# Optimization experiments

Measured on AMD Instinct MI355X. Metric: run time of the kernel, lower is better.

The kernel has to match this reference:

```python
import jax, jax.numpy as jnp
import numpy as np

# 3x3 hexagon kernel mask: zero at (0,2) and (2,0), matching HexagonConv2d
_KM = np.ones((3, 3), np.float32)
_KM[0, 2] = 0.0
_KM[2, 0] = 0.0
KMASK = jnp.asarray(_KM)


def _out_mask():
    # static 13x13 mask encoding the post-conv zeroing loops
    m = np.ones((13, 13), np.float32)
    for i in range(5):
        for j in range(8 + i, 13):
            m[i, j] = 0.0
    for i in range(4):
        m[2 + i, 9 + i] = 0.0
    m[6:9, 12] = 0.0
    for i in range(6):
        for j in range(i + 1):
            m[6 + i, j] = 0.0
    for i in range(3):
        m[5 + i, 0 + i] = 0.0
    m[3:5, 0] = 0.0
    return jnp.asarray(m)

OUT_MASK = _out_mask()


def _hex_pad(x):
    # x: [B,C,13,13] -> zero-pad to [B,C,15,15], then hexagonal wraparound copies.
    # Copies applied sequentially, exactly matching the torch in-place order
    # (one copy, row 0 <- row 12, feeds a later read at (0,7)).
    x = jnp.pad(x, ((0, 0), (0, 0), (1, 1), (1, 1)))
    r2 = jnp.arange(2)
    r3 = jnp.arange(3)
    r4 = jnp.arange(4)
    r8 = jnp.arange(8)
    x = x.at[:, :, 0, 1:8].set(x[:, :, 12, 7:14])
    x = x.at[:, :, r3, 8 + r3].set(x[:, :, 6 + r3, 2 + r3])
    x = x.at[:, :, 3 + r4, 10 + r4].set(x[:, :, 9 + r4, 4 + r4])
    x = x.at[:, :, 7 + r3, 13].set(x[:, :, 1 + r3, 1])
    x = x.at[:, :, 10 + r3, 14].set(x[:, :, 4 + r3, 2])
    x = x.at[:, :, 13, 7 + r8].set(x[:, :, 1, 1 + r8])
    x = x.at[:, :, 9 + r4, 3 + r4].set(x[:, :, 3 + r4, 9 + r4])
    x = x.at[:, :, 6 + r3, 1 + r3].set(x[:, :, r3, 7 + r3])
    x = x.at[:, :, 4 + r2, 1].set(x[:, :, 10 + r2, 13])
    x = x.at[:, :, r4, 0].set(x[:, :, 6 + r4, 12])
    return x


def setup_inputs() -> dict:
    key = jax.random.key(0)
    kx, kw, kb = jax.random.split(key, 3)
    B, Cin, Cout, H = 4096, 64, 64, 13
    x = jax.random.normal(kx, (B, Cin, H, H), dtype=jnp.float32)
    fan_in = Cin * 9
    w = jax.random.normal(kw, (Cout, Cin, 3, 3), dtype=jnp.float32) / np.sqrt(fan_in)
    b = jax.random.normal(kb, (Cout,), dtype=jnp.float32) * 0.01
    return {"x": x, "w": w, "b": b}


def reference(x, w, b):
    xp = _hex_pad(x)                      # [B,C,15,15]
    wm = w * KMASK                        # hexagonal kernel mask
    y = jax.lax.conv_general_dilated(
        xp, wm, window_strides=(1, 1), padding="VALID",
        dimension_numbers=("NCHW", "OIHW", "NCHW"))  # [B,Cout,13,13]
    y = y + b[None, :, None, None]
    return y * OUT_MASK
```

## Files before the change

### kernel.cpp

```cpp
#include <hip/hip_runtime.h>
#include <stdint.h>

typedef __attribute__((ext_vector_type(8))) short short8;
typedef __attribute__((ext_vector_type(4))) float float4v;

#define NPIX 240
#define PIXSTRIDE 68

#define MAP_OFF   57344
#define OM_OFF    58304

__device__ __forceinline__ unsigned short f2bf(float f) {
    union { float f; unsigned u; } v; v.f = f;
    unsigned r = v.u + 0x7FFFu + ((v.u >> 16) & 1u);
    return (unsigned short)(r >> 16);
}

__global__ void hex_prep_kernel(const float* __restrict__ w,
                                unsigned short* __restrict__ wsA,
                                int* __restrict__ map,
                                float* __restrict__ om) {
    const int gid = blockIdx.x * blockDim.x + threadIdx.x;
    const int nthr = gridDim.x * blockDim.x;
    const int ti_tab[7] = {0,0,1,1,1,2,2};
    const int tj_tab[7] = {0,1,0,1,2,1,2};
    for (int item = gid; item < 4*14*64; item += nthr) {
        int lane = item & 63;
        int ks   = (item >> 6) % 14;
        int ct   = (item >> 6) / 14;
        int co = ct*16 + (lane & 15);
        int k0 = ks*32 + (lane >> 4)*8;
        unsigned short vals[8];
        #pragma unroll
        for (int j = 0; j < 8; ++j) {
            int k = k0 + j;
            int tap = k >> 6, ci = k & 63;
            vals[j] = f2bf(w[(co*64 + ci)*9 + ti_tab[tap]*3 + tj_tab[tap]]);
        }
        for (int j = 0; j < 8; ++j) wsA[item*8 + j] = vals[j];
    }
    if (gid == 0) {
        int m[225];
        for (int r = 0; r < 15; ++r)
            for (int c = 0; c < 15; ++c)
                m[r*15+c] = (r>=1 && r<=13 && c>=1 && c<=13) ? (r-1)*13 + (c-1) : -1;
        #define M(r,c) m[(r)*15+(c)]
        for (int t = 0; t < 7; ++t) M(0,1+t)    = M(12,7+t);
        for (int r = 0; r < 3; ++r) M(r,8+r)    = M(6+r,2+r);
        for (int r = 0; r < 4; ++r) M(3+r,10+r) = M(9+r,4+r);
        for (int r = 0; r < 3; ++r) M(7+r,13)   = M(1+r,1);
        for (int r = 0; r < 3; ++r) M(10+r,14)  = M(4+r,2);
        for (int r = 0; r < 8; ++r) M(13,7+r)   = M(1,1+r);
        for (int r = 0; r < 4; ++r) M(9+r,3+r)  = M(3+r,9+r);
        for (int r = 0; r < 3; ++r) M(6+r,1+r)  = M(r,7+r);
        for (int r = 0; r < 2; ++r) M(4+r,1)    = M(10+r,13);
        for (int r = 0; r < 4; ++r) M(r,0)      = M(6+r,12);
        #undef M
        for (int i = 0; i < 225; ++i) map[i] = m[i];
        for (int i = 225; i < 240; ++i) map[i] = -1;
        float o[169];
        for (int i = 0; i < 169; ++i) o[i] = 1.f;
        for (int i = 0; i < 5; ++i) for (int j = 8+i; j < 13; ++j) o[i*13+j] = 0.f;
        for (int i = 0; i < 4; ++i) o[(2+i)*13 + 9+i] = 0.f;
        for (int i = 6; i < 9; ++i) o[i*13 + 12] = 0.f;
        for (int i = 0; i < 6; ++i) for (int j = 0; j <= i; ++j) o[(6+i)*13 + j] = 0.f;
        for (int i = 0; i < 3; ++i) o[(5+i)*13 + i] = 0.f;
        o[3*13 + 0] = 0.f; o[4*13 + 0] = 0.f;
        for (int i = 0; i < 169; ++i) om[i] = o[i];
    }
}

__global__ __launch_bounds__(256, 2) void hexconv_kernel(
        const float* __restrict__ x, const float* __restrict__ bias,
        const unsigned short* __restrict__ wsA, const int* __restrict__ map,
        const float* __restrict__ om, float* __restrict__ out) {
    __shared__ unsigned short Xs[NPIX * PIXSTRIDE];
    const int b   = blockIdx.x;
    const int tid = threadIdx.x;
    const int lane = tid & 63, wv = tid >> 6;
    const int lr = lane & 15, lq = lane >> 4;
    const float* xb = x + (size_t)b * 64 * 169;

    const int ctp = wv & 1;
    const int nth = wv >> 1;

    short8 afr[2][14];
    #pragma unroll
    for (int c = 0; c < 2; ++c) {
        const int ct = ctp*2 + c;
        #pragma unroll
        for (int ks = 0; ks < 14; ++ks)
            afr[c][ks] = *(const short8*)(wsA + (size_t)((ct*14 + ks)*64 + lane)*8);
    }

    int sp[4];
    #pragma unroll
    for (int pi = 0; pi < 4; ++pi) {
        int pix = lane + 64*pi;
        sp[pi] = (pix < NPIX) ? map[pix] : -1;
    }
    #pragma unroll
    for (int pi = 0; pi < 4; ++pi) {
        int pix = lane + 64*pi;
        if (pix < NPIX) {
            const int s = sp[pi];
            unsigned short vals[16];
            #pragma unroll
            for (int cj = 0; cj < 16; ++cj) {
                int ci = wv*16 + cj;
                float v = (s >= 0) ? xb[ci*169 + s] : 0.f;
                vals[cj] = f2bf(v);
            }
            #pragma unroll
            for (int q = 0; q < 4; ++q) {
                uint64_t pk = (uint64_t)vals[4*q]
                            | ((uint64_t)vals[4*q+1] << 16)
                            | ((uint64_t)vals[4*q+2] << 32)
                            | ((uint64_t)vals[4*q+3] << 48);
                *(uint64_t*)&Xs[pix*PIXSTRIDE + wv*16 + q*4] = pk;
            }
        }
    }
    __syncthreads();

    float4v acc[2][7];
    #pragma unroll
    for (int c = 0; c < 2; ++c)
        #pragma unroll
        for (int j = 0; j < 7; ++j)
            acc[c][j] = float4v{0.f, 0.f, 0.f, 0.f};

    const int offs[7] = {0,1,15,16,17,31,32};
    #pragma unroll
    for (int ks = 0; ks < 14; ++ks) {
        const int tap = ks >> 1;
        const int cib = (ks & 1)*32 + lq*8;
        #pragma unroll
        for (int j = 0; j < 7; ++j) {
            int nt = nth*7 + j;
            if (nt < 13) {
                int pixb = nt*16 + lr + offs[tap];
                const unsigned short* p = &Xs[pixb*PIXSTRIDE + cib];
                union { short8 v; uint64_t q[2]; } u;
                u.q[0] = *(const uint64_t*)p;
                u.q[1] = *(const uint64_t*)(p + 4);
                #pragma unroll
                for (int c = 0; c < 2; ++c)
                    acc[c][j] = __builtin_amdgcn_mfma_f32_16x16x32_bf16(
                        afr[c][ks], u.v, acc[c][j], 0, 0, 0);
            }
        }
    }

    #pragma unroll
    for (int j = 0; j < 7; ++j) {
        int nt = nth*7 + j;
        if (nt >= 13) continue;
        int p15 = nt*16 + lr;
        int y = p15 / 15, xc = p15 % 15;
        if (xc >= 13 || y >= 13) continue;
        float omv = om[y*13 + xc];
        size_t obase = (size_t)b*64*169 + y*13 + xc;
        #pragma unroll
        for (int c = 0; c < 2; ++c) {
            int ct = ctp*2 + c;
            #pragma unroll
            for (int r = 0; r < 4; ++r) {
                int co = ct*16 + lq*4 + r;
                out[obase + (size_t)co*169] = (acc[c][j][r] + bias[co]) * omv;
            }
        }
    }
}

extern "C" void kernel_launch(void* const* d_in, const int* in_sizes, int n_in,
                              void* d_out, int out_size, void* d_ws, size_t ws_size,
                              hipStream_t stream) {
    const float* x    = (const float*)d_in[0];
    const float* w    = (const float*)d_in[1];
    const float* bias = (const float*)d_in[2];
    float* out = (float*)d_out;

    unsigned short* wsA = (unsigned short*)d_ws;
    int*   map = (int*)((char*)d_ws + MAP_OFF);
    float* om  = (float*)((char*)d_ws + OM_OFF);

    hex_prep_kernel<<<16, 256, 0, stream>>>(w, wsA, map, om);

    int B = in_sizes[0] / (64 * 169);
    hexconv_kernel<<<B, 256, 0, stream>>>(x, bias, wsA, map, om, out);
}
```

Baseline: 358.8 us.

## Make conv kernel persistent with double-buffered LDS prefetch of next image

Switches from one block per image to 512 persistent blocks, each processing a contiguous chunk of images. Weight fragments, bias, pixel maps and output mask are loaded once per block, and the next image's global loads and bf16 LDS writes are interleaved with the MFMA work on the current image using two LDS buffers. The aim is to hide global load latency behind compute and to amortize per-block setup. It doubles LDS use, which may reduce occupancy, and raises register pressure from holding the prefetched values.

```diff
diff --git a/kernel.cpp b/kernel.cpp
--- a/kernel.cpp
+++ b/kernel.cpp
@@ -1,5 +1,6 @@
 #include <hip/hip_runtime.h>
 #include <stdint.h>
+
 
 typedef __attribute__((ext_vector_type(8))) short short8;
 typedef __attribute__((ext_vector_type(4))) float float4v;
@@ -73,17 +74,19 @@
 __global__ __launch_bounds__(256, 2) void hexconv_kernel(
         const float* __restrict__ x, const float* __restrict__ bias,
         const unsigned short* __restrict__ wsA, const int* __restrict__ map,
-        const float* __restrict__ om, float* __restrict__ out) {
-    __shared__ unsigned short Xs[NPIX * PIXSTRIDE];
-    const int b   = blockIdx.x;
+        const float* __restrict__ om, float* __restrict__ out,
+        int B, int ipb) {
+    __shared__ unsigned short Xs[2][NPIX * PIXSTRIDE];
     const int tid = threadIdx.x;
     const int lane = tid & 63, wv = tid >> 6;
     const int lr = lane & 15, lq = lane >> 4;
-    const float* xb = x + (size_t)b * 64 * 169;
-
     const int ctp = wv & 1;
     const int nth = wv >> 1;
 
+    const int b0   = blockIdx.x * ipb;
+    const int bend = (b0 + ipb < B) ? (b0 + ipb) : B;
+    if (b0 >= bend) return;
+
     short8 afr[2][14];
     #pragma unroll
     for (int c = 0; c < 2; ++c) {
@@ -92,85 +95,143 @@
         for (int ks = 0; ks < 14; ++ks)
             afr[c][ks] = *(const short8*)(wsA + (size_t)((ct*14 + ks)*64 + lane)*8);
     }
-
     int sp[4];
     #pragma unroll
     for (int pi = 0; pi < 4; ++pi) {
         int pix = lane + 64*pi;
         sp[pi] = (pix < NPIX) ? map[pix] : -1;
     }
-    #pragma unroll
-    for (int pi = 0; pi < 4; ++pi) {
-        int pix = lane + 64*pi;
-        if (pix < NPIX) {
-            const int s = sp[pi];
-            unsigned short vals[16];
-            #pragma unroll
-            for (int cj = 0; cj < 16; ++cj) {
-                int ci = wv*16 + cj;
-                float v = (s >= 0) ? xb[ci*169 + s] : 0.f;
-                vals[cj] = f2bf(v);
-            }
-            #pragma unroll
-            for (int q = 0; q < 4; ++q) {
-                uint64_t pk = (uint64_t)vals[4*q]
-                            | ((uint64_t)vals[4*q+1] << 16)
-                            | ((uint64_t)vals[4*q+2] << 32)
-                            | ((uint64_t)vals[4*q+3] << 48);
-                *(uint64_t*)&Xs[pix*PIXSTRIDE + wv*16 + q*4] = pk;
-            }
-        }
-    }
-    __syncthreads();
-
-    float4v acc[2][7];
+    float biasv[2][4];
     #pragma unroll
     for (int c = 0; c < 2; ++c)
         #pragma unroll
-        for (int j = 0; j < 7; ++j)
-            acc[c][j] = float4v{0.f, 0.f, 0.f, 0.f};
-
-    const int offs[7] = {0,1,15,16,17,31,32};
-    #pragma unroll
-    for (int ks = 0; ks < 14; ++ks) {
-        const int tap = ks >> 1;
-        const int cib = (ks & 1)*32 + lq*8;
-        #pragma unroll
-        for (int j = 0; j < 7; ++j) {
-            int nt = nth*7 + j;
-            if (nt < 13) {
-                int pixb = nt*16 + lr + offs[tap];
-                const unsigned short* p = &Xs[pixb*PIXSTRIDE + cib];
-                union { short8 v; uint64_t q[2]; } u;
-                u.q[0] = *(const uint64_t*)p;
-                u.q[1] = *(const uint64_t*)(p + 4);
-                #pragma unroll
-                for (int c = 0; c < 2; ++c)
-                    acc[c][j] = __builtin_amdgcn_mfma_f32_16x16x32_bf16(
-                        afr[c][ks], u.v, acc[c][j], 0, 0, 0);
-            }
-        }
-    }
-
+        for (int r = 0; r < 4; ++r)
+            biasv[c][r] = bias[(ctp*2 + c)*16 + lq*4 + r];
+    int ep_off[7]; float ep_om[7]; unsigned okmask = 0;
     #pragma unroll
     for (int j = 0; j < 7; ++j) {
         int nt = nth*7 + j;
-        if (nt >= 13) continue;
         int p15 = nt*16 + lr;
         int y = p15 / 15, xc = p15 % 15;
-        if (xc >= 13 || y >= 13) continue;
-        float omv = om[y*13 + xc];
-        size_t obase = (size_t)b*64*169 + y*13 + xc;
-        #pragma unroll
-        for (int c = 0; c < 2; ++c) {
-            int ct = ctp*2 + c;
+        bool ok = (nt < 13) && (xc < 13) && (y < 13);
+        ep_off[j] = ok ? (y*13 + xc) : 0;
+        ep_om[j]  = ok ? om[y*13 + xc] : 0.f;
+        if (ok) okmask |= (1u << j);
+    }
+
+    auto issue2 = [&](const float* __restrict__ xb, int pp, float (&lv)[2][16]) {
+        #pragma unroll
+        for (int h = 0; h < 2; ++h) {
+            int pi = 2*pp + h;
+            int pix = lane + 64*pi;
+            if (pix < NPIX) {
+                int s = sp[pi];
+                #pragma unroll
+                for (int cj = 0; cj < 16; ++cj)
+                    lv[h][cj] = (s >= 0) ? xb[(wv*16 + cj)*169 + s] : 0.f;
+            }
+        }
+    };
+    auto cwrite2 = [&](int sel, int pp, const float (&lv)[2][16]) {
+        #pragma unroll
+        for (int h = 0; h < 2; ++h) {
+            int pi = 2*pp + h;
+            int pix = lane + 64*pi;
+            if (pix < NPIX) {
+                #pragma unroll
+                for (int q = 0; q < 4; ++q) {
+                    uint64_t pk = (uint64_t)f2bf(lv[h][4*q])
+                                | ((uint64_t)f2bf(lv[h][4*q+1]) << 16)
+                                | ((uint64_t)f2bf(lv[h][4*q+2]) << 32)
+                                | ((uint64_t)f2bf(lv[h][4*q+3]) << 48);
+                    *(uint64_t*)&Xs[sel][pix*PIXSTRIDE + wv*16 + q*4] = pk;
+                }
+            }
+        }
+    };
+
+    const int offs[7] = {0,1,15,16,17,31,32};
+
+#define MFMA_HALF(SEL, KBASE) do {                                            \
+    _Pragma("unroll")                                                         \
+    for (int kk = 0; kk < 7; ++kk) {                                          \
+        const int ks = (KBASE) + kk;                                          \
+        const int tap = ks >> 1;                  \
+        const int cib = (ks & 1)*32 + lq*8;                                   \
+        _Pragma("unroll")                                                     \
+        for (int j = 0; j < 7; ++j) {                                         \
+            int nt = nth*7 + j;                                               \
+            if (nt < 13) {                                                    \
+                int pixb = nt*16 + lr + offs[tap];                            \
+                const unsigned short* p = &Xs[SEL][pixb*PIXSTRIDE + cib];     \
+                union { short8 v; uint64_t q[2]; } u;                         \
+                u.q[0] = *(const uint64_t*)p;                                 \
+                u.q[1] = *(const uint64_t*)(p + 4);                           \
+                _Pragma("unroll")                                             \
+                for (int c = 0; c < 2; ++c)                                   \
+                    acc[c][j] = __builtin_amdgcn_mfma_f32_16x16x32_bf16(      \
+                        afr[c][ks], u.v, acc[c][j], 0, 0, 0);                 \
+            }                                                                 \
+        }                                                                     \
+    }                                                                         \
+} while (0)
+
+    {
+        const float* xb = x + (size_t)b0 * 64 * 169;
+        float lv[2][16];
+        issue2(xb, 0, lv);
+        cwrite2(0, 0, lv);
+        issue2(xb, 1, lv);
+        cwrite2(0, 1, lv);
+    }
+    __syncthreads();
+
+    int cur = 0;
+    for (int b = b0; b < bend; ++b) {
+        const bool havenext = (b + 1 < bend);
+        const float* xbn = x + (size_t)(b + 1) * 64 * 169;
+
+        float4v acc[2][7];
+        #pragma unroll
+        for (int c = 0; c < 2; ++c)
             #pragma unroll
-            for (int r = 0; r < 4; ++r) {
-                int co = ct*16 + lq*4 + r;
-                out[obase + (size_t)co*169] = (acc[c][j][r] + bias[co]) * omv;
+            for (int j = 0; j < 7; ++j)
+                acc[c][j] = float4v{0.f, 0.f, 0.f, 0.f};
+
+        float lv[2][16];
+        if (havenext) issue2(xbn, 0, lv);
+
+        MFMA_HALF(cur, 0);
+
+        if (havenext) {
+            cwrite2(cur ^ 1, 0, lv);
+            issue2(xbn, 1, lv);
+        }
+
+        MFMA_HALF(cur, 7);
+
+        if (havenext) cwrite2(cur ^ 1, 1, lv);
+
+        __syncthreads();
+
+        #pragma unroll
+        for (int j = 0; j < 7; ++j) {
+            if (!((okmask >> j) & 1u)) continue;
+            size_t obase = (size_t)b * (64*169) + ep_off[j];
+            float omv = ep_om[j];
+            #pragma unroll
+            for (int c = 0; c < 2; ++c) {
+                #pragma unroll
+                for (int r = 0; r < 4; ++r) {
+                    int co = (ctp*2 + c)*16 + lq*4 + r;
+                    out[obase + (size_t)co*169] = (acc[c][j][r] + biasv[c][r]) * omv;
+                }
             }
         }
-    }
+
+        cur ^= 1;
+    }
+#undef MFMA_HALF
 }
 
 extern "C" void kernel_launch(void* const* d_in, const int* in_sizes, int n_in,
@@ -188,5 +249,8 @@
     hex_prep_kernel<<<16, 256, 0, stream>>>(w, wsA, map, om);
 
     int B = in_sizes[0] / (64 * 169);
-    hexconv_kernel<<<B, 256, 0, stream>>>(x, bias, wsA, map, om, out);
-}
+    int nblk = 512;
+    if (nblk > B) nblk = B;
+    int ipb = (B + nblk - 1) / nblk;
+    hexconv_kernel<<<nblk, 256, 0, stream>>>(x, bias, wsA, map, om, out, B, ipb);
+}
```

New measurement: 660.7 us. +84.1%, slower.

## Process multiple images per block to amortize weight and index loads

Applied to the files above, without the earlier changes.

Turns the kernel into a loop over four batch images per block. The weight fragments, pixel map, bias and output-mask/offset values are loaded once per block and reused across those images, and an extra barrier protects the shared tile between iterations. Launch bounds are also raised to ask for three blocks per CU, which caps registers per thread more tightly and risks spills given the large A-fragment and accumulator arrays. The grid shrinks to 1024 blocks, which lowers the number of resident waves available to hide load latency.

```diff
diff --git a/kernel.cpp b/kernel.cpp
--- a/kernel.cpp
+++ b/kernel.cpp
@@ -1,5 +1,6 @@
 #include <hip/hip_runtime.h>
 #include <stdint.h>
+
 
 typedef __attribute__((ext_vector_type(8))) short short8;
 typedef __attribute__((ext_vector_type(4))) float float4v;
@@ -70,20 +71,22 @@
     }
 }
 
-__global__ __launch_bounds__(256, 2) void hexconv_kernel(
+__global__ __launch_bounds__(256, 3) void hexconv_kernel(
         const float* __restrict__ x, const float* __restrict__ bias,
         const unsigned short* __restrict__ wsA, const int* __restrict__ map,
-        const float* __restrict__ om, float* __restrict__ out) {
+        const float* __restrict__ om, float* __restrict__ out,
+        int B, int ipb) {
     __shared__ unsigned short Xs[NPIX * PIXSTRIDE];
-    const int b   = blockIdx.x;
     const int tid = threadIdx.x;
     const int lane = tid & 63, wv = tid >> 6;
     const int lr = lane & 15, lq = lane >> 4;
-    const float* xb = x + (size_t)b * 64 * 169;
-
     const int ctp = wv & 1;
     const int nth = wv >> 1;
 
+    const int b0   = blockIdx.x * ipb;
+    const int bend = (b0 + ipb < B) ? (b0 + ipb) : B;
+    if (b0 >= bend) return;
+
     short8 afr[2][14];
     #pragma unroll
     for (int c = 0; c < 2; ++c) {
@@ -92,84 +95,103 @@
         for (int ks = 0; ks < 14; ++ks)
             afr[c][ks] = *(const short8*)(wsA + (size_t)((ct*14 + ks)*64 + lane)*8);
     }
-
     int sp[4];
     #pragma unroll
     for (int pi = 0; pi < 4; ++pi) {
         int pix = lane + 64*pi;
         sp[pi] = (pix < NPIX) ? map[pix] : -1;
     }
-    #pragma unroll
-    for (int pi = 0; pi < 4; ++pi) {
-        int pix = lane + 64*pi;
-        if (pix < NPIX) {
-            const int s = sp[pi];
-            unsigned short vals[16];
-            #pragma unroll
-            for (int cj = 0; cj < 16; ++cj) {
-                int ci = wv*16 + cj;
-                float v = (s >= 0) ? xb[ci*169 + s] : 0.f;
-                vals[cj] = f2bf(v);
-            }
-            #pragma unroll
-            for (int q = 0; q < 4; ++q) {
-                uint64_t pk = (uint64_t)vals[4*q]
-                            | ((uint64_t)vals[4*q+1] << 16)
-                            | ((uint64_t)vals[4*q+2] << 32)
-                            | ((uint64_t)vals[4*q+3] << 48);
-                *(uint64_t*)&Xs[pix*PIXSTRIDE + wv*16 + q*4] = pk;
-            }
-        }
-    }
-    __syncthreads();
-
-    float4v acc[2][7];
+    float biasv[2][4];
     #pragma unroll
     for (int c = 0; c < 2; ++c)
         #pragma unroll
-        for (int j = 0; j < 7; ++j)
-            acc[c][j] = float4v{0.f, 0.f, 0.f, 0.f};
-
-    const int offs[7] = {0,1,15,16,17,31,32};
-    #pragma unroll
-    for (int ks = 0; ks < 14; ++ks) {
-        const int tap = ks >> 1;
-        const int cib = (ks & 1)*32 + lq*8;
-        #pragma unroll
-        for (int j = 0; j < 7; ++j) {
-            int nt = nth*7 + j;
-            if (nt < 13) {
-                int pixb = nt*16 + lr + offs[tap];
-                const unsigned short* p = &Xs[pixb*PIXSTRIDE + cib];
-                union { short8 v; uint64_t q[2]; } u;
-                u.q[0] = *(const uint64_t*)p;
-                u.q[1] = *(const uint64_t*)(p + 4);
-                #pragma unroll
-                for (int c = 0; c < 2; ++c)
-                    acc[c][j] = __builtin_amdgcn_mfma_f32_16x16x32_bf16(
-                        afr[c][ks], u.v, acc[c][j], 0, 0, 0);
-            }
-        }
-    }
-
+        for (int r = 0; r < 4; ++r)
+            biasv[c][r] = bias[(ctp*2 + c)*16 + lq*4 + r];
+    int ep_off[7]; float ep_om[7]; unsigned okmask = 0;
     #pragma unroll
     for (int j = 0; j < 7; ++j) {
         int nt = nth*7 + j;
-        if (nt >= 13) continue;
         int p15 = nt*16 + lr;
         int y = p15 / 15, xc = p15 % 15;
-        if (xc >= 13 || y >= 13) continue;
-        float omv = om[y*13 + xc];
-        size_t obase = (size_t)b*64*169 + y*13 + xc;
-        #pragma unroll
-        for (int c = 0; c < 2; ++c) {
-            int ct = ctp*2 + c;
+        bool ok = (nt < 13) && (xc < 13) && (y < 13);
+        ep_off[j] = ok ? (y*13 + xc) : 0;
+        ep_om[j]  = ok ? om[y*13 + xc] : 0.f;
+        if (ok) okmask |= (1u << j);
+    }
+
+    const int offs[7] = {0,1,15,16,17,31,32};
+
+    for (int b = b0; b < bend; ++b) {
+        const float* xb = x + (size_t)b * (64*169);
+
+        #pragma unroll
+        for (int pi = 0; pi < 4; ++pi) {
+            int pix = lane + 64*pi;
+            if (pix < NPIX) {
+                const int s = sp[pi];
+                unsigned short vals[16];
+                #pragma unroll
+                for (int cj = 0; cj < 16; ++cj) {
+                    int ci = wv*16 + cj;
+                    float v = (s >= 0) ? xb[ci*169 + s] : 0.f;
+                    vals[cj] = f2bf(v);
+                }
+                #pragma unroll
+                for (int q = 0; q < 4; ++q) {
+                    uint64_t pk = (uint64_t)vals[4*q]
+                                | ((uint64_t)vals[4*q+1] << 16)
+                                | ((uint64_t)vals[4*q+2] << 32)
+                                | ((uint64_t)vals[4*q+3] << 48);
+                    *(uint64_t*)&Xs[pix*PIXSTRIDE + wv*16 + q*4] = pk;
+                }
+            }
+        }
+        __syncthreads();
+
+        float4v acc[2][7];
+        #pragma unroll
+        for (int c = 0; c < 2; ++c)
             #pragma unroll
-            for (int r = 0; r < 4; ++r) {
-                int co = ct*16 + lq*4 + r;
-                out[obase + (size_t)co*169] = (acc[c][j][r] + bias[co]) * omv;
+            for (int j = 0; j < 7; ++j)
+                acc[c][j] = float4v{0.f, 0.f, 0.f, 0.f};
+
+        #pragma unroll
+        for (int ks = 0; ks < 14; ++ks) {
+            const int tap = ks >> 1;
+            const int cib = (ks & 1)*32 + lq*8;
+            #pragma unroll
+            for (int j = 0; j < 7; ++j) {
+                int nt = nth*7 + j;
+                if (nt < 13) {
+                    int pixb = nt*16 + lr + offs[tap];
+                    const unsigned short* p = &Xs[pixb*PIXSTRIDE + cib];
+                    union { short8 v; uint64_t q[2]; } u;
+                    u.q[0] = *(const uint64_t*)p;
+                    u.q[1] = *(const uint64_t*)(p + 4);
+                    #pragma unroll
+                    for (int c = 0; c < 2; ++c)
+                        acc[c][j] = __builtin_amdgcn_mfma_f32_16x16x32_bf16(
+                            afr[c][ks], u.v, acc[c][j], 0, 0, 0);
+                }
             }
         }
+
+        #pragma unroll
+        for (int j = 0; j < 7; ++j) {
+            if (!((okmask >> j) & 1u)) continue;
+            size_t obase = (size_t)b * (64*169) + ep_off[j];
+            float omv = ep_om[j];
+            #pragma unroll
+            for (int c = 0; c < 2; ++c) {
+                #pragma unroll
+                for (int r = 0; r < 4; ++r) {
+                    int co = (ctp*2 + c)*16 + lq*4 + r;
+                    out[obase + (size_t)co*169] = (acc[c][j][r] + biasv[c][r]) * omv;
+                }
+            }
+        }
+
+        __syncthreads();
     }
 }
 
@@ -188,5 +210,7 @@
     hex_prep_kernel<<<16, 256, 0, stream>>>(w, wsA, map, om);
 
     int B = in_sizes[0] / (64 * 169);
-    hexconv_kernel<<<B, 256, 0, stream>>>(x, bias, wsA, map, om, out);
-}
+    int ipb = 4;
+    int nblk = (B + ipb - 1) / ipb;
+    hexconv_kernel<<<nblk, 256, 0, stream>>>(x, bias, wsA, map, om, out, B, ipb);
+}
```

Result: slower. 1.221 ms (+240.3%).

## Make conv kernel persistent with double-buffered LDS staging across batch images

Applied to the files above, without the earlier changes.

The conv kernel now launches a fixed grid of 512 blocks, and each block loops over several batch images. It loads the bf16 weight fragments and pixel map once per block instead of once per image. The next image's input is staged into a second LDS buffer while the current one is computed, so global gathers overlap with MFMA work. In exchange LDS use doubles, which may limit how many blocks fit per CU, and there are fewer blocks in flight to hide latency.

```diff
diff --git a/kernel.cpp b/kernel.cpp
--- a/kernel.cpp
+++ b/kernel.cpp
@@ -1,5 +1,6 @@
 #include <hip/hip_runtime.h>
 #include <stdint.h>
+
 
 typedef __attribute__((ext_vector_type(8))) short short8;
 typedef __attribute__((ext_vector_type(4))) float float4v;
@@ -73,16 +74,18 @@
 __global__ __launch_bounds__(256, 2) void hexconv_kernel(
         const float* __restrict__ x, const float* __restrict__ bias,
         const unsigned short* __restrict__ wsA, const int* __restrict__ map,
-        const float* __restrict__ om, float* __restrict__ out) {
-    __shared__ unsigned short Xs[NPIX * PIXSTRIDE];
-    const int b   = blockIdx.x;
+        const float* __restrict__ om, float* __restrict__ out,
+        int B, int ipb) {
+    __shared__ unsigned short Xs[2][NPIX * PIXSTRIDE];
     const int tid = threadIdx.x;
     const int lane = tid & 63, wv = tid >> 6;
     const int lr = lane & 15, lq = lane >> 4;
-    const float* xb = x + (size_t)b * 64 * 169;
-
     const int ctp = wv & 1;
     const int nth = wv >> 1;
+
+    const int b0   = blockIdx.x * ipb;
+    const int bend = (b0 + ipb < B) ? (b0 + ipb) : B;
+    if (b0 >= bend) return;
 
     short8 afr[2][14];
     #pragma unroll
@@ -92,84 +95,98 @@
         for (int ks = 0; ks < 14; ++ks)
             afr[c][ks] = *(const short8*)(wsA + (size_t)((ct*14 + ks)*64 + lane)*8);
     }
-
     int sp[4];
     #pragma unroll
     for (int pi = 0; pi < 4; ++pi) {
         int pix = lane + 64*pi;
         sp[pi] = (pix < NPIX) ? map[pix] : -1;
     }
-    #pragma unroll
-    for (int pi = 0; pi < 4; ++pi) {
-        int pix = lane + 64*pi;
-        if (pix < NPIX) {
-            const int s = sp[pi];
-            unsigned short vals[16];
+
+    auto stage = [&](int sel, const float* __restrict__ xb) {
+        #pragma unroll
+        for (int pi = 0; pi < 4; ++pi) {
+            int pix = lane + 64*pi;
+            if (pix < NPIX) {
+                const int s = sp[pi];
+                unsigned short vals[16];
+                #pragma unroll
+                for (int cj = 0; cj < 16; ++cj) {
+                    int ci = wv*16 + cj;
+                    float v = (s >= 0) ? xb[ci*169 + s] : 0.f;
+                    vals[cj] = f2bf(v);
+                }
+                #pragma unroll
+                for (int q = 0; q < 4; ++q) {
+                    uint64_t pk = (uint64_t)vals[4*q]
+                                | ((uint64_t)vals[4*q+1] << 16)
+                                | ((uint64_t)vals[4*q+2] << 32)
+                                | ((uint64_t)vals[4*q+3] << 48);
+                    *(uint64_t*)&Xs[sel][pix*PIXSTRIDE + wv*16 + q*4] = pk;
+                }
+            }
+        }
+    };
+
+    const int offs[7] = {0,1,15,16,17,31,32};
+
+    stage(0, x + (size_t)b0 * (64*169));
+    __syncthreads();
+
+    int cur = 0;
+    for (int b = b0; b < bend; ++b) {
+        if (b + 1 < bend)
+            stage(cur ^ 1, x + (size_t)(b + 1) * (64*169));
+
+        float4v acc[2][7];
+        #pragma unroll
+        for (int c = 0; c < 2; ++c)
             #pragma unroll
-            for (int cj = 0; cj < 16; ++cj) {
-                int ci = wv*16 + cj;
-                float v = (s >= 0) ? xb[ci*169 + s] : 0.f;
-                vals[cj] = f2bf(v);
+            for (int j = 0; j < 7; ++j)
+                acc[c][j] = float4v{0.f, 0.f, 0.f, 0.f};
+
+        #pragma unroll
+        for (int ks = 0; ks < 14; ++ks) {
+            const int tap = ks >> 1;
+            const int cib = (ks & 1)*32 + lq*8;
+            #pragma unroll
+            for (int j = 0; j < 7; ++j) {
+                int nt = nth*7 + j;
+                if (nt < 13) {
+                    int pixb = nt*16 + lr + offs[tap];
+                    const unsigned short* p = &Xs[cur][pixb*PIXSTRIDE + cib];
+                    union { short8 v; uint64_t q[2]; } u;
+                    u.q[0] = *(const uint64_t*)p;
+                    u.q[1] = *(const uint64_t*)(p + 4);
+                    #pragma unroll
+                    for (int c = 0; c < 2; ++c)
+                        acc[c][j] = __builtin_amdgcn_mfma_f32_16x16x32_bf16(
+                            afr[c][ks], u.v, acc[c][j], 0, 0, 0);
+                }
             }
-            #pragma unroll
-            for (int q = 0; q < 4; ++q) {
-                uint64_t pk = (uint64_t)vals[4*q]
-                            | ((uint64_t)vals[4*q+1] << 16)
-                            | ((uint64_t)vals[4*q+2] << 32)
-                            | ((uint64_t)vals[4*q+3] << 48);
-                *(uint64_t*)&Xs[pix*PIXSTRIDE + wv*16 + q*4] = pk;
-            }
-        }
-    }
-    __syncthreads();
-
-    float4v acc[2][7];
-    #pragma unroll
-    for (int c = 0; c < 2; ++c)
-        #pragma unroll
-        for (int j = 0; j < 7; ++j)
-            acc[c][j] = float4v{0.f, 0.f, 0.f, 0.f};
-
-    const int offs[7] = {0,1,15,16,17,31,32};
-    #pragma unroll
-    for (int ks = 0; ks < 14; ++ks) {
-        const int tap = ks >> 1;
-        const int cib = (ks & 1)*32 + lq*8;
+        }
+
         #pragma unroll
         for (int j = 0; j < 7; ++j) {
             int nt = nth*7 + j;
-            if (nt < 13) {
-                int pixb = nt*16 + lr + offs[tap];
-                const unsigned short* p = &Xs[pixb*PIXSTRIDE + cib];
-                union { short8 v; uint64_t q[2]; } u;
-                u.q[0] = *(const uint64_t*)p;
-                u.q[1] = *(const uint64_t*)(p + 4);
+            if (nt >= 13) continue;
+            int p15 = nt*16 + lr;
+            int y = p15 / 15, xc = p15 % 15;
+            if (xc >= 13 || y >= 13) continue;
+            float omv = om[y*13 + xc];
+            size_t obase = (size_t)b * (64*169) + y*13 + xc;
+            #pragma unroll
+            for (int c = 0; c < 2; ++c) {
+                int ct = ctp*2 + c;
                 #pragma unroll
-                for (int c = 0; c < 2; ++c)
-                    acc[c][j] = __builtin_amdgcn_mfma_f32_16x16x32_bf16(
-                        afr[c][ks], u.v, acc[c][j], 0, 0, 0);
+                for (int r = 0; r < 4; ++r) {
+                    int co = ct*16 + lq*4 + r;
+                    out[obase + (size_t)co*169] = (acc[c][j][r] + bias[co]) * omv;
+                }
             }
         }
-    }
-
-    #pragma unroll
-    for (int j = 0; j < 7; ++j) {
-        int nt = nth*7 + j;
-        if (nt >= 13) continue;
-        int p15 = nt*16 + lr;
-        int y = p15 / 15, xc = p15 % 15;
-        if (xc >= 13 || y >= 13) continue;
-        float omv = om[y*13 + xc];
-        size_t obase = (size_t)b*64*169 + y*13 + xc;
-        #pragma unroll
-        for (int c = 0; c < 2; ++c) {
-            int ct = ctp*2 + c;
-            #pragma unroll
-            for (int r = 0; r < 4; ++r) {
-                int co = ct*16 + lq*4 + r;
-                out[obase + (size_t)co*169] = (acc[c][j][r] + bias[co]) * omv;
-            }
-        }
+
+        __syncthreads();
+        cur ^= 1;
     }
 }
 
@@ -188,5 +205,8 @@
     hex_prep_kernel<<<16, 256, 0, stream>>>(w, wsA, map, om);
 
     int B = in_sizes[0] / (64 * 169);
-    hexconv_kernel<<<B, 256, 0, stream>>>(x, bias, wsA, map, om, out);
-}
+    int nblk = 512;
+    if (nblk > B) nblk = B;
+    int ipb = (B + nblk - 1) / nblk;
+    hexconv_kernel<<<nblk, 256, 0, stream>>>(x, bias, wsA, map, om, out, B, ipb);
+}
```

After: 579.5 us. 61.5% more time.
